# Performance work log

Measured on AMD Instinct MI355X. Metric: run time of the kernel, lower is better.

## Reference

```python
import jax, jax.numpy as jnp
import numpy as np

D_MODEL = 1024
D_HEAD = 64

def setup_inputs() -> dict:
    key = jax.random.key(0)
    kx, kk, kq, kv = jax.random.split(key, 4)
    s = D_MODEL ** -0.5
    return {
        "x": jax.random.normal(kx, (4, 4096, D_MODEL), dtype=jnp.float32),
        "Wk": jax.random.normal(kk, (D_MODEL, D_HEAD), dtype=jnp.float32) * s,
        "Wq": jax.random.normal(kq, (D_MODEL, D_HEAD), dtype=jnp.float32) * s,
        "Wv": jax.random.normal(kv, (D_MODEL, D_HEAD), dtype=jnp.float32) * s,
    }

def reference(x, Wk, Wq, Wv):
    # x: [B, T, d_model]; Wk/Wq/Wv: [d_model, d_head]
    B, T, _ = x.shape
    d_head = Wk.shape[1]
    k = x @ Wk  # [B, T, d_head]
    q = x @ Wq
    v = x @ Wv
    scores = jnp.einsum("btd,bsd->bts", q, k) * (d_head ** -0.5)  # [B, T, T]
    causal = jnp.tril(jnp.ones((T, T), dtype=bool))
    scores = jnp.where(causal, scores, -jnp.inf)
    weights = jax.nn.softmax(scores, axis=-1)
    return jnp.einsum("bts,bsd->btd", weights, v)
```

## Files before the change

### kernel.cpp

```cpp
#include <hip/hip_runtime.h>

typedef __attribute__((ext_vector_type(8))) short bf16x8;
typedef __attribute__((ext_vector_type(4))) float f32x4;

#define DI __device__ __forceinline__

DI unsigned short f2bf(float f) {
    unsigned int u = __builtin_bit_cast(unsigned int, f);
    u += 0x7fff + ((u >> 16) & 1);
    return (unsigned short)(u >> 16);
}

DI unsigned int cvtpk(float lo, float hi) {
    unsigned int r;
    asm("v_cvt_pk_bf16_f32 %0, %1, %2" : "=v"(r) : "v"(lo), "v"(hi));
    return r;
}

DI float fexp2(float x) {
    float r;
    asm("v_exp_f32 %0, %1" : "=v"(r) : "v"(x));
    return r;
}

DI void gl_lds16(const void* g, void* l) {
    __builtin_amdgcn_global_load_lds(
        (const __attribute__((address_space(1))) unsigned int*)g,
        (__attribute__((address_space(3))) unsigned int*)l, 16, 0, 0);
}

#define WAITCNT(n) asm volatile("s_waitcnt vmcnt(" #n ")" ::: "memory")

__global__ __launch_bounds__(256) void wt_kernel(
    const float* __restrict__ Wk, const float* __restrict__ Wq,
    const float* __restrict__ Wv, unsigned short* __restrict__ Wt)
{
    __shared__ float ws[64][65];
    const int m = blockIdx.x >> 4, kc = blockIdx.x & 15;
    const float* W = (m == 0) ? Wq : (m == 1) ? Wk : Wv;
    const float scale = (m == 0) ? 0.18033688011112042f : 1.0f;
    const int tid = threadIdx.x;
    #pragma unroll
    for (int r = 0; r < 16; ++r) {
        int idx = r * 256 + tid;
        ws[idx >> 6][idx & 63] = W[(kc * 64 + (idx >> 6)) * 64 + (idx & 63)] * scale;
    }
    __syncthreads();
    const int c = tid >> 2, k4 = (tid & 3) * 16;
    bf16x8 o0, o1;
    #pragma unroll
    for (int j = 0; j < 8; ++j) o0[j] = (short)f2bf(ws[k4 + j][c]);
    #pragma unroll
    for (int j = 0; j < 8; ++j) o1[j] = (short)f2bf(ws[k4 + 8 + j][c]);
    unsigned short* dst = Wt + ((size_t)m * 64 + c) * 1024 + kc * 64 + k4;
    *(bf16x8*)dst = o0;
    *(bf16x8*)(dst + 8) = o1;
}

__global__ __launch_bounds__(256) void proj_kernel(
    const float* __restrict__ x, const unsigned short* __restrict__ Wt,
    unsigned short* __restrict__ qw, unsigned short* __restrict__ kw,
    unsigned short* __restrict__ vT)
{
    __shared__ char LDSx[3][8192];
    __shared__ char LDSb[3][6144];

    const int tid = threadIdx.x;
    const int w = tid >> 6, l = tid & 63;
    const int xr = l & 15, lg = l >> 4;
    const int rb = blockIdx.x & 255, ch = blockIdx.x >> 8;
    const int row0 = rb * 64;

    const char* xsrc = (const char*)x + (size_t)row0 * 4096;
    const char* Wtb = (const char*)Wt;

    const int xrow_l = l >> 3, xcb = (l & 7) * 16;
    const int brow_l = l >> 2, bcb = (l & 3) * 16;

    auto stage = [&](int nb, int s) {
        #pragma unroll
        for (int c = 0; c < 4; ++c) {
            const int ci = w + 4 * c;
            if (ci < 8) {
                const int row = ci * 8 + xrow_l;
                const int sw = (row & 7) << 4;
                gl_lds16(xsrc + (size_t)row * 4096 + (size_t)s * 128 + (xcb ^ sw),
                         LDSx[nb] + ci * 1024);
            } else if (ci < 14) {
                const int c8 = ci - 8;
                const int r = c8 * 16 + brow_l;
                const int sw = ((r >> 1) & 3) << 4;
                const int wtrow = (r >> 5) * 64 + ch * 32 + (r & 31);
                gl_lds16(Wtb + (size_t)wtrow * 2048 + (size_t)s * 64 + (bcb ^ sw),
                         LDSb[nb] + c8 * 1024);
            }
        }
    };

    f32x4 acc[3][2];
    #pragma unroll
    for (int m = 0; m < 3; ++m)
        #pragma unroll
        for (int tt = 0; tt < 2; ++tt) { f32x4 z = {0.f,0.f,0.f,0.f}; acc[m][tt] = z; }

    const int Rw = w * 16 + xr;
    const int swx = (Rw & 7) << 4;

    auto compute = [&](int pb) {
        float4 va = *(const float4*)(LDSx[pb] + Rw * 128 + ((32 * lg) ^ swx));
        float4 vb = *(const float4*)(LDSx[pb] + Rw * 128 + ((32 * lg + 16) ^ swx));
        uint4 au;
        au.x = cvtpk(va.x, va.y); au.y = cvtpk(va.z, va.w);
        au.z = cvtpk(vb.x, vb.y); au.w = cvtpk(vb.z, vb.w);
        bf16x8 a = __builtin_bit_cast(bf16x8, au);
        __builtin_amdgcn_s_setprio(1);
        #pragma unroll
        for (int m = 0; m < 3; ++m)
            #pragma unroll
            for (int tt = 0; tt < 2; ++tt) {
                const int rB = m * 32 + tt * 16 + xr;
                bf16x8 bfr = *(const bf16x8*)(LDSb[pb] + rB * 64 +
                                ((16 * lg) ^ (((rB >> 1) & 3) << 4)));
                acc[m][tt] = __builtin_amdgcn_mfma_f32_16x16x32_bf16(a, bfr, acc[m][tt], 0, 0, 0);
            }
        __builtin_amdgcn_s_setprio(0);
    };

    stage(0, 0); stage(1, 1);

    int cb = 0, nb = 2;
    for (int s = 0; s < 32; ++s) {
        if (s == 31) { WAITCNT(0); }
        else if (w < 2) { WAITCNT(4); }
        else { WAITCNT(3); }
        __builtin_amdgcn_sched_barrier(0);
        __builtin_amdgcn_s_barrier();
        if (s + 2 < 32) stage(nb, s + 2);
        compute(cb);
        cb = (cb == 2) ? 0 : cb + 1;
        nb = (nb == 2) ? 0 : nb + 1;
    }

    const int bb = row0 >> 12;
    #pragma unroll
    for (int tt = 0; tt < 2; ++tt) {
        const int col = ch * 32 + tt * 16 + xr;
        #pragma unroll
        for (int i = 0; i < 4; ++i) {
            const int grow = row0 + w * 16 + 4 * lg + i;
            qw[(size_t)grow * 64 + col] = f2bf(acc[0][tt][i]);
            kw[(size_t)grow * 64 + col] = f2bf(acc[1][tt][i]);
        }
        uint2 pv;
        pv.x = cvtpk(acc[2][tt][0], acc[2][tt][1]);
        pv.y = cvtpk(acc[2][tt][2], acc[2][tt][3]);
        const int lr0 = (row0 & 4095) + w * 16 + 4 * lg;
        *(uint2*)&vT[((size_t)bb * 64 + col) * 4096 + lr0] = pv;
    }
}

__global__ __launch_bounds__(256) void attn_kernel(
    const unsigned short* __restrict__ qw, const unsigned short* __restrict__ kw,
    const unsigned short* __restrict__ vT,
    unsigned short* __restrict__ POb, float* __restrict__ Pl)
{
    __shared__ __align__(16) unsigned short Kb[2][4096];
    __shared__ __align__(16) unsigned short Vb[2][4096];
    __shared__ __align__(16) unsigned short Ps[4][16][64];

    const int id = blockIdx.x;
    const int qb = 63 - (id & 63);
    const int b  = (id >> 6) & 3;
    const int c  = id >> 8;
    if (c * 8 > qb) return;

    const int tid = threadIdx.x;
    const int w = tid >> 6, l = tid & 63;
    const int xr = l & 15, g = l >> 4;

    const int t0 = c * 8;
    const int rem0 = qb + 1 - t0;
    const int tcnt = rem0 < 8 ? rem0 : 8;
    const size_t base = (size_t)b * 4096;
    const int qrow = qb * 64 + w * 16;
    const int myrow = qrow + xr;

    bf16x8 aq[2];
    #pragma unroll
    for (int h = 0; h < 2; ++h)
        aq[h] = *(const bf16x8*)(qw + (base + myrow) * 64 + 32 * h + 8 * g);

    const int wo0 = w * 2048, wo1 = wo0 + 1024;
    const int o0 = wo0 + 16 * l, o1 = wo1 + 16 * l;
    const int k0sw = (o0 & ~127) | ((o0 & 127) ^ (((o0 >> 7) & 7) << 4));
    const int k1sw = (o1 & ~127) | ((o1 & 127) ^ (((o1 >> 7) & 7) << 4));
    const size_t v0sw = (size_t)(o0 >> 7) * 8192 + ((o0 & 127) ^ (((o0 >> 7) & 7) << 4));
    const size_t v1sw = (size_t)(o1 >> 7) * 8192 + ((o1 & 127) ^ (((o1 >> 7) & 7) << 4));
    const char* kwb  = (const char*)kw + base * 128;
    const char* vtb0 = (const char*)vT + (size_t)b * 64 * 8192;

    auto stage = [&](int bi, int it) {
        const char* kt = kwb + (size_t)it * 8192;
        gl_lds16(kt + k0sw, (char*)Kb[bi] + wo0);
        gl_lds16(kt + k1sw, (char*)Kb[bi] + wo1);
        const char* vt = vtb0 + (size_t)it * 128;
        gl_lds16(vt + v0sw, (char*)Vb[bi] + wo0);
        gl_lds16(vt + v1sw, (char*)Vb[bi] + wo1);
    };

    f32x4 accO[4];
    #pragma unroll
    for (int t = 0; t < 4; ++t) { f32x4 z = {0.f,0.f,0.f,0.f}; accO[t] = z; }
    float lsum = 0.f;

    const int swz = (xr & 7) << 4;
    char* const psrow = (char*)Ps + w * 2048 + xr * 128;

    stage(0, t0);
    if (tcnt > 1) stage(1, t0 + 1);

    for (int tt = 0; tt < tcnt; ++tt) {
        const int it = t0 + tt;
        const int bi = tt & 1;
        if (tt + 1 < tcnt) { WAITCNT(4); } else { WAITCNT(0); }
        __builtin_amdgcn_sched_barrier(0);
        __builtin_amdgcn_s_barrier();

        const char* kbase = (const char*)Kb[bi];
        f32x4 s[4];
        __builtin_amdgcn_s_setprio(1);
        #pragma unroll
        for (int t = 0; t < 4; ++t) {
            f32x4 z = {0.f,0.f,0.f,0.f};
            s[t] = z;
            #pragma unroll
            for (int h = 0; h < 2; ++h) {
                bf16x8 ak = *(const bf16x8*)(kbase + (xr + 16 * t) * 128 + ((64 * h + 16 * g) ^ swz));
                s[t] = __builtin_amdgcn_mfma_f32_16x16x32_bf16(ak, aq[h], s[t], 0, 0, 0);
            }
        }
        __builtin_amdgcn_s_setprio(0);

        if (it == qb) {
            #pragma unroll
            for (int t = 0; t < 4; ++t)
                #pragma unroll
                for (int i = 0; i < 4; ++i) {
                    const int key = it * 64 + 16 * t + 4 * g + i;
                    if (key > myrow) s[t][i] = -1e30f;
                }
        }

        #pragma unroll
        for (int t = 0; t < 4; ++t)
            #pragma unroll
            for (int i = 0; i < 4; ++i) {
                float v = s[t][i];
                s[t][i] = fexp2(v);
            }

        {
            float a0 = (s[0][0] + s[0][1]) + (s[0][2] + s[0][3]);
            float a1 = (s[1][0] + s[1][1]) + (s[1][2] + s[1][3]);
            float a2 = (s[2][0] + s[2][1]) + (s[2][2] + s[2][3]);
            float a3 = (s[3][0] + s[3][1]) + (s[3][2] + s[3][3]);
            lsum += (a0 + a1) + (a2 + a3);
        }

        #pragma unroll
        for (int t = 0; t < 4; ++t) {
            uint2 uu;
            uu.x = cvtpk(s[t][0], s[t][1]);
            uu.y = cvtpk(s[t][2], s[t][3]);
            *(uint2*)(psrow + ((32 * t + 8 * g) ^ swz)) = uu;
        }

        bf16x8 pa[2];
        #pragma unroll
        for (int h = 0; h < 2; ++h)
            pa[h] = *(const bf16x8*)(psrow + ((16 * g + 64 * h) ^ swz));
        const char* vbase = (const char*)Vb[bi];
        __builtin_amdgcn_s_setprio(1);
        #pragma unroll
        for (int t = 0; t < 4; ++t)
            #pragma unroll
            for (int h = 0; h < 2; ++h) {
                bf16x8 av = *(const bf16x8*)(vbase + (16 * t + xr) * 128 + ((64 * h + 16 * g) ^ swz));
                accO[t] = __builtin_amdgcn_mfma_f32_16x16x32_bf16(av, pa[h], accO[t], 0, 0, 0);
            }
        __builtin_amdgcn_s_setprio(0);

        __builtin_amdgcn_s_barrier();
        if (tt + 2 < tcnt) stage(bi, it + 2);
    }

    lsum += __shfl_xor(lsum, 16, 64);
    lsum += __shfl_xor(lsum, 32, 64);

    const size_t prow = (size_t)(b * 8 + c) * 4096 + qrow;
    #pragma unroll
    for (int t = 0; t < 4; ++t) {
        uint2 uu;
        uu.x = cvtpk(accO[t][0], accO[t][1]);
        uu.y = cvtpk(accO[t][2], accO[t][3]);
        *(uint2*)&POb[(prow + xr) * 64 + 16 * t + 4 * g] = uu;
    }
    if (l < 16) Pl[prow + l] = lsum;
}

__global__ __launch_bounds__(256) void merge_kernel(
    const unsigned short* __restrict__ POb, const float* __restrict__ Pl,
    float* __restrict__ out)
{
    const int gid = blockIdx.x * 256 + threadIdx.x;
    const int r = gid >> 3;
    const int c0 = (gid & 7) * 8;
    const int b = r >> 12, lr = r & 4095;
    const int nc = (lr >> 9) + 1;

    float L = 0.f;
    #pragma unroll
    for (int ci = 0; ci < 8; ++ci)
        if (ci < nc) L += Pl[(size_t)(b * 8 + ci) * 4096 + lr];
    const float rL = 1.0f / L;

    float acc[8];
    #pragma unroll
    for (int j = 0; j < 8; ++j) acc[j] = 0.f;

    #pragma unroll
    for (int ci = 0; ci < 8; ++ci) {
        if (ci < nc) {
            const unsigned short* p = POb + ((size_t)(b * 8 + ci) * 4096 + lr) * 64 + c0;
            uint4 u = *(const uint4*)p;
            const unsigned int us[4] = {u.x, u.y, u.z, u.w};
            #pragma unroll
            for (int k = 0; k < 4; ++k) {
                acc[2 * k]     += __builtin_bit_cast(float, us[k] << 16);
                acc[2 * k + 1] += __builtin_bit_cast(float, us[k] & 0xFFFF0000u);
            }
        }
    }
    float* op = out + (size_t)r * 64 + c0;
    float4 v0, v1;
    v0.x = acc[0] * rL; v0.y = acc[1] * rL; v0.z = acc[2] * rL; v0.w = acc[3] * rL;
    v1.x = acc[4] * rL; v1.y = acc[5] * rL; v1.z = acc[6] * rL; v1.w = acc[7] * rL;
    *(float4*)op = v0;
    *(float4*)(op + 4) = v1;
}

extern "C" void kernel_launch(void* const* d_in, const int* in_sizes, int n_in,
                              void* d_out, int out_size, void* d_ws, size_t ws_size,
                              hipStream_t stream) {
    const float* x  = (const float*)d_in[0];
    const float* Wk = (const float*)d_in[1];
    const float* Wq = (const float*)d_in[2];
    const float* Wv = (const float*)d_in[3];
    float* out = (float*)d_out;

    char* wsb = (char*)d_ws;
    unsigned short* POb = (unsigned short*)wsb;
    float* Pl = (float*)(wsb + (size_t)17 * 1024 * 1024);
    unsigned short* Wt = (unsigned short*)(wsb + (size_t)24 * 1024 * 1024);
    unsigned short* qw = Wt + (size_t)3 * 64 * 1024;
    unsigned short* kw = qw + (size_t)16384 * 64;
    unsigned short* vT = kw + (size_t)16384 * 64;

    hipLaunchKernelGGL(wt_kernel, dim3(48), dim3(256), 0, stream, Wk, Wq, Wv, Wt);
    hipLaunchKernelGGL(proj_kernel, dim3(512), dim3(256), 0, stream, x, Wt, qw, kw, vT);
    hipLaunchKernelGGL(attn_kernel, dim3(2048), dim3(256), 0, stream, qw, kw, vT, POb, Pl);
    hipLaunchKernelGGL(merge_kernel, dim3(512), dim3(256), 0, stream, POb, Pl, out);
}
```

Baseline: 59.29 us.

## Use 32x32 MFMA tiles with 128-row query blocks and permlane P transpose

The attention kernel moves from 16x16x32 to 32x32x16 bf16 MFMA. Each block now covers 128 query rows (32 per wave), and the grid is halved. The P tile is turned into the A operand in registers with v_permlane32_swap rather than a round trip through shared memory. This removes LDS traffic and barriers for P and doubles K/V reuse per staged tile, but raises register pressure and leaves fewer, coarser blocks, which may hurt load balance on the causal triangle.

```diff
diff --git a/kernel.cpp b/kernel.cpp
--- a/kernel.cpp
+++ b/kernel.cpp
@@ -2,6 +2,7 @@
 
 typedef __attribute__((ext_vector_type(8))) short bf16x8;
 typedef __attribute__((ext_vector_type(4))) float f32x4;
+typedef __attribute__((ext_vector_type(16))) float f32x16;
 
 #define DI __device__ __forceinline__
 
@@ -166,29 +167,29 @@
 {
     __shared__ __align__(16) unsigned short Kb[2][4096];
     __shared__ __align__(16) unsigned short Vb[2][4096];
-    __shared__ __align__(16) unsigned short Ps[4][16][64];
 
     const int id = blockIdx.x;
-    const int qb = 63 - (id & 63);
-    const int b  = (id >> 6) & 3;
-    const int c  = id >> 8;
-    if (c * 8 > qb) return;
+    const int qb = 31 - (id & 31);
+    const int b  = (id >> 5) & 3;
+    const int c  = id >> 7;
+    if (c * 4 > qb) return;
 
     const int tid = threadIdx.x;
     const int w = tid >> 6, l = tid & 63;
-    const int xr = l & 15, g = l >> 4;
+    const int q32 = l & 31, h = l >> 5;
 
     const int t0 = c * 8;
-    const int rem0 = qb + 1 - t0;
+    const int ntt = 2 * qb + 2;
+    const int rem0 = ntt - t0;
     const int tcnt = rem0 < 8 ? rem0 : 8;
     const size_t base = (size_t)b * 4096;
-    const int qrow = qb * 64 + w * 16;
-    const int myrow = qrow + xr;
-
-    bf16x8 aq[2];
-    #pragma unroll
-    for (int h = 0; h < 2; ++h)
-        aq[h] = *(const bf16x8*)(qw + (base + myrow) * 64 + 32 * h + 8 * g);
+    const int qrow0 = qb * 128 + w * 32;
+    const int myrow = qrow0 + q32;
+
+    bf16x8 aq[4];
+    #pragma unroll
+    for (int c16 = 0; c16 < 4; ++c16)
+        aq[c16] = *(const bf16x8*)(qw + (base + myrow) * 64 + 16 * c16 + 8 * h);
 
     const int wo0 = w * 2048, wo1 = wo0 + 1024;
     const int o0 = wo0 + 16 * l, o1 = wo1 + 16 * l;
@@ -208,13 +209,12 @@
         gl_lds16(vt + v1sw, (char*)Vb[bi] + wo1);
     };
 
-    f32x4 accO[4];
-    #pragma unroll
-    for (int t = 0; t < 4; ++t) { f32x4 z = {0.f,0.f,0.f,0.f}; accO[t] = z; }
+    f32x16 accO[2];
+    #pragma unroll
+    for (int dt = 0; dt < 2; ++dt)
+        #pragma unroll
+        for (int r = 0; r < 16; ++r) accO[dt][r] = 0.f;
     float lsum = 0.f;
-
-    const int swz = (xr & 7) << 4;
-    char* const psrow = (char*)Ps + w * 2048 + xr * 128;
 
     stage(0, t0);
     if (tcnt > 1) stage(1, t0 + 1);
@@ -227,85 +227,96 @@
         __builtin_amdgcn_s_barrier();
 
         const char* kbase = (const char*)Kb[bi];
-        f32x4 s[4];
+        f32x16 s2[2];
+        #pragma unroll
+        for (int kt = 0; kt < 2; ++kt)
+            #pragma unroll
+            for (int r = 0; r < 16; ++r) s2[kt][r] = 0.f;
         __builtin_amdgcn_s_setprio(1);
         #pragma unroll
-        for (int t = 0; t < 4; ++t) {
-            f32x4 z = {0.f,0.f,0.f,0.f};
-            s[t] = z;
-            #pragma unroll
-            for (int h = 0; h < 2; ++h) {
-                bf16x8 ak = *(const bf16x8*)(kbase + (xr + 16 * t) * 128 + ((64 * h + 16 * g) ^ swz));
-                s[t] = __builtin_amdgcn_mfma_f32_16x16x32_bf16(ak, aq[h], s[t], 0, 0, 0);
+        for (int kt = 0; kt < 2; ++kt) {
+            const int row = 32 * kt + q32;
+            const int sw = (row & 7) << 4;
+            #pragma unroll
+            for (int c16 = 0; c16 < 4; ++c16) {
+                bf16x8 ak = *(const bf16x8*)(kbase + row * 128 + ((32 * c16 + 16 * h) ^ sw));
+                s2[kt] = __builtin_amdgcn_mfma_f32_32x32x16_bf16(ak, aq[c16], s2[kt], 0, 0, 0);
             }
         }
         __builtin_amdgcn_s_setprio(0);
 
-        if (it == qb) {
-            #pragma unroll
-            for (int t = 0; t < 4; ++t)
+        if (it >= 2 * qb) {
+            #pragma unroll
+            for (int kt = 0; kt < 2; ++kt)
                 #pragma unroll
-                for (int i = 0; i < 4; ++i) {
-                    const int key = it * 64 + 16 * t + 4 * g + i;
-                    if (key > myrow) s[t][i] = -1e30f;
+                for (int r = 0; r < 16; ++r) {
+                    const int key = it * 64 + 32 * kt + (r & 3) + 8 * (r >> 2) + 4 * h;
+                    if (key > myrow) s2[kt][r] = -1e30f;
                 }
         }
 
         #pragma unroll
-        for (int t = 0; t < 4; ++t)
-            #pragma unroll
-            for (int i = 0; i < 4; ++i) {
-                float v = s[t][i];
-                s[t][i] = fexp2(v);
-            }
-
-        {
-            float a0 = (s[0][0] + s[0][1]) + (s[0][2] + s[0][3]);
-            float a1 = (s[1][0] + s[1][1]) + (s[1][2] + s[1][3]);
-            float a2 = (s[2][0] + s[2][1]) + (s[2][2] + s[2][3]);
-            float a3 = (s[3][0] + s[3][1]) + (s[3][2] + s[3][3]);
-            lsum += (a0 + a1) + (a2 + a3);
-        }
-
-        #pragma unroll
-        for (int t = 0; t < 4; ++t) {
-            uint2 uu;
-            uu.x = cvtpk(s[t][0], s[t][1]);
-            uu.y = cvtpk(s[t][2], s[t][3]);
-            *(uint2*)(psrow + ((32 * t + 8 * g) ^ swz)) = uu;
-        }
-
-        bf16x8 pa[2];
-        #pragma unroll
-        for (int h = 0; h < 2; ++h)
-            pa[h] = *(const bf16x8*)(psrow + ((16 * g + 64 * h) ^ swz));
+        for (int kt = 0; kt < 2; ++kt)
+            #pragma unroll
+            for (int r = 0; r < 16; ++r) {
+                float v = fexp2(s2[kt][r]);
+                s2[kt][r] = v;
+                lsum += v;
+            }
+
+        bf16x8 pa[4];
+        #pragma unroll
+        for (int kt = 0; kt < 2; ++kt) {
+            unsigned ua[8];
+            #pragma unroll
+            for (int q2 = 0; q2 < 4; ++q2) {
+                ua[2 * q2]     = cvtpk(s2[kt][4 * q2],     s2[kt][4 * q2 + 1]);
+                ua[2 * q2 + 1] = cvtpk(s2[kt][4 * q2 + 2], s2[kt][4 * q2 + 3]);
+            }
+            #pragma unroll
+            for (int e = 0; e < 2; ++e) {
+                unsigned x0 = ua[4 * e + 0], x1 = ua[4 * e + 1];
+                unsigned y0 = ua[4 * e + 2], y1 = ua[4 * e + 3];
+                asm("v_permlane32_swap_b32 %0, %1" : "+v"(x0), "+v"(y0));
+                asm("v_permlane32_swap_b32 %0, %1" : "+v"(x1), "+v"(y1));
+                uint4 pu;
+                pu.x = x0; pu.y = x1; pu.z = y0; pu.w = y1;
+                pa[2 * kt + e] = __builtin_bit_cast(bf16x8, pu);
+            }
+        }
+
         const char* vbase = (const char*)Vb[bi];
         __builtin_amdgcn_s_setprio(1);
         #pragma unroll
-        for (int t = 0; t < 4; ++t)
-            #pragma unroll
-            for (int h = 0; h < 2; ++h) {
-                bf16x8 av = *(const bf16x8*)(vbase + (16 * t + xr) * 128 + ((64 * h + 16 * g) ^ swz));
-                accO[t] = __builtin_amdgcn_mfma_f32_16x16x32_bf16(av, pa[h], accO[t], 0, 0, 0);
-            }
+        for (int dt = 0; dt < 2; ++dt) {
+            const int row = 32 * dt + q32;
+            const int sw = (row & 7) << 4;
+            #pragma unroll
+            for (int kc = 0; kc < 4; ++kc) {
+                bf16x8 av = *(const bf16x8*)(vbase + row * 128 + ((32 * kc + 16 * h) ^ sw));
+                accO[dt] = __builtin_amdgcn_mfma_f32_32x32x16_bf16(av, pa[kc], accO[dt], 0, 0, 0);
+            }
+        }
         __builtin_amdgcn_s_setprio(0);
 
         __builtin_amdgcn_s_barrier();
         if (tt + 2 < tcnt) stage(bi, it + 2);
     }
 
-    lsum += __shfl_xor(lsum, 16, 64);
     lsum += __shfl_xor(lsum, 32, 64);
 
-    const size_t prow = (size_t)(b * 8 + c) * 4096 + qrow;
-    #pragma unroll
-    for (int t = 0; t < 4; ++t) {
-        uint2 uu;
-        uu.x = cvtpk(accO[t][0], accO[t][1]);
-        uu.y = cvtpk(accO[t][2], accO[t][3]);
-        *(uint2*)&POb[(prow + xr) * 64 + 16 * t + 4 * g] = uu;
-    }
-    if (l < 16) Pl[prow + l] = lsum;
+    const size_t prow = (size_t)(b * 8 + c) * 4096 + qrow0;
+    #pragma unroll
+    for (int dt = 0; dt < 2; ++dt)
+        #pragma unroll
+        for (int q2 = 0; q2 < 4; ++q2) {
+            uint2 uu;
+            uu.x = cvtpk(accO[dt][4 * q2],     accO[dt][4 * q2 + 1]);
+            uu.y = cvtpk(accO[dt][4 * q2 + 2], accO[dt][4 * q2 + 3]);
+            const int d = 32 * dt + 8 * q2 + 4 * h;
+            *(uint2*)&POb[(prow + q32) * 64 + d] = uu;
+        }
+    if (l < 32) Pl[prow + l] = lsum;
 }
 
 __global__ __launch_bounds__(256) void merge_kernel(
@@ -368,6 +379,6 @@
 
     hipLaunchKernelGGL(wt_kernel, dim3(48), dim3(256), 0, stream, Wk, Wq, Wv, Wt);
     hipLaunchKernelGGL(proj_kernel, dim3(512), dim3(256), 0, stream, x, Wt, qw, kw, vT);
-    hipLaunchKernelGGL(attn_kernel, dim3(2048), dim3(256), 0, stream, qw, kw, vT, POb, Pl);
+    hipLaunchKernelGGL(attn_kernel, dim3(1024), dim3(256), 0, stream, qw, kw, vT, POb, Pl);
     hipLaunchKernelGGL(merge_kernel, dim3(512), dim3(256), 0, stream, POb, Pl, out);
 }
```

Measured after the change: 63.13 us. 6.5% more time.
